# Performance work log

Hardware: AMD Instinct MI355X
Metric: run time of the kernel (lower is better)

The kernel has to match this reference:

```python
import jax, jax.numpy as jnp
import numpy as np

N_NODES = 3000
N_FEAT = 2
N_UNITS = 64
BATCH = 16
K_DIFF = 2  # max_diffusion_step


def _supports(adj):
    # dual_random_walk: (D^-1 A)^T and (D'^-1 A^T)^T, rows with zero degree -> 0
    def rw_T(A):
        d = A.sum(axis=1)
        d_inv = jnp.where(d > 0, 1.0 / d, 0.0)
        return (d_inv[:, None] * A).T  # (N, N)
    return [rw_T(adj), rw_T(adj.T)]


def _gconv(inputs, state, supports, W, b, num_nodes):
    # inputs: (B, N*F), state: (B, N*U)
    B = inputs.shape[0]
    x = jnp.concatenate([inputs.reshape(B, num_nodes, -1),
                         state.reshape(B, num_nodes, -1)], axis=2)  # (B, N, C)
    x0 = x.transpose(1, 2, 0)  # (N, C, B)
    mats = [x0]
    for S in supports:
        x1 = jnp.einsum('mn,ncb->mcb', S, x0)
        mats.append(x1)
        xk_1, xk_2 = x1, x0
        for _ in range(2, K_DIFF + 1):
            x2 = 2.0 * jnp.einsum('mn,ncb->mcb', S, xk_1) - xk_2  # Chebyshev recurrence
            mats.append(x2)
            xk_1, xk_2 = x2, xk_1
    xs = jnp.stack(mats, axis=0)  # (M, N, C, B)
    M, _, C, _ = xs.shape
    xs = xs.transpose(3, 1, 2, 0).reshape(B * num_nodes, C * M)
    out = xs @ W + b  # (B*N, O)
    return out.reshape(B, num_nodes * W.shape[1])


def setup_inputs() -> dict:
    key = jax.random.key(0)
    k1, k2, k3, k4, k5 = jax.random.split(key, 5)
    C = N_FEAT + N_UNITS          # 66
    M = 2 * K_DIFF + 1            # 5 (two supports)
    xw = lambda k, s: jax.random.normal(k, s, dtype=jnp.float32) * jnp.sqrt(2.0 / (s[0] + s[1]))
    return {
        "inputs": jax.random.normal(k1, (BATCH, N_NODES * N_FEAT), dtype=jnp.float32),
        "hx": jax.random.normal(k2, (BATCH, N_NODES * N_UNITS), dtype=jnp.float32),
        "adj_mx": jax.random.uniform(k3, (N_NODES, N_NODES), dtype=jnp.float32),
        "W_gate": xw(k4, (C * M, 2 * N_UNITS)),
        "b_gate": jnp.ones((2 * N_UNITS,), dtype=jnp.float32),  # bias_start=1.0
        "W_cand": xw(k5, (C * M, N_UNITS)),
        "b_cand": jnp.zeros((N_UNITS,), dtype=jnp.float32),
        "num_nodes": N_NODES,
    }


def reference(inputs, hx, adj_mx, W_gate, b_gate, W_cand, b_cand, num_nodes):
    supports = _supports(adj_mx)
    B = inputs.shape[0]
    value = jax.nn.sigmoid(_gconv(inputs, hx, supports, W_gate, b_gate, num_nodes))
    value = value.reshape(B, num_nodes, 2 * N_UNITS)
    r, u = value[..., :N_UNITS], value[..., N_UNITS:]
    r = r.reshape(B, num_nodes * N_UNITS)
    u = u.reshape(B, num_nodes * N_UNITS)
    c = jnp.tanh(_gconv(inputs, r * hx, supports, W_cand, b_cand, num_nodes))
    new_state = u * hx + (1.0 - u) * c
    return new_state
```

## Files before the change

kernel.cpp:

```cpp
#include <hip/hip_runtime.h>
#include <cstdint>
#include <cstddef>


typedef unsigned short u16;
typedef __bf16 bf16x8 __attribute__((ext_vector_type(8)));
typedef u16 u16x8 __attribute__((ext_vector_type(8)));
typedef float f32x4 __attribute__((ext_vector_type(4)));

#define NND 3000
#define KP  3008
#define NBX 16
#define NCB 1056
#define KW  330
#define KWP 352

__device__ __forceinline__ float b2f(u16 x) { return (float)__builtin_bit_cast(__bf16, x); }
__device__ __forceinline__ u16 f2b(float f) { return __builtin_bit_cast(u16, (__bf16)f); }

__device__ __forceinline__ void gll16(const u16* g, void* l) {
  __builtin_amdgcn_global_load_lds(
      (const __attribute__((address_space(1))) unsigned int*)g,
      (__attribute__((address_space(3))) unsigned int*)l, 16, 0, 0);
}


__global__ void k_probe(const u16* __restrict__ bg, int* __restrict__ flag) {
  if (threadIdx.x == 0 && blockIdx.x == 0) *flag = (bg[0] == 0x3F80) ? 0 : 1;
}

__device__ __forceinline__ float rdf(const void* p, size_t i, int mode) {
  return mode ? ((const float*)p)[i] : b2f(((const u16*)p)[i]);
}


__global__ __launch_bounds__(256) void k_rowsum(const void* __restrict__ A, float* __restrict__ d0inv,
                                                const int* __restrict__ flag) {
  const int row = blockIdx.x, t = threadIdx.x;
  const int mode = *flag;
  float s = 0.f;
  if (mode) {
    const float* a = (const float*)A + (size_t)row * NND;
    for (int j = t; j < NND; j += 256) s += a[j];
  } else {
    const u16* a = (const u16*)A + (size_t)row * NND;
    for (int j = t; j < NND; j += 256) s += b2f(a[j]);
  }
  for (int off = 32; off; off >>= 1) s += __shfl_down(s, off, 64);
  __shared__ float red[4];
  if ((t & 63) == 0) red[t >> 6] = s;
  __syncthreads();
  if (t == 0) {
    float tot = red[0] + red[1] + red[2] + red[3];
    d0inv[row] = tot > 0.f ? 1.f / tot : 0.f;
  }
}

__global__ __launch_bounds__(256) void k_colsum(const void* __restrict__ A, float* __restrict__ d1sum,
                                                const int* __restrict__ flag) {
  const int j = blockIdx.x * 256 + threadIdx.x;
  if (j >= NND) return;
  const int mode = *flag;
  const int i0 = blockIdx.y * 100;
  float s = 0.f;
  if (mode) {
    const float* a = (const float*)A;
    for (int i = i0; i < i0 + 100; ++i) s += a[(size_t)i * NND + j];
  } else {
    const u16* a = (const u16*)A;
    for (int i = i0; i < i0 + 100; ++i) s += b2f(a[(size_t)i * NND + j]);
  }
  atomicAdd(&d1sum[j], s);
}

__global__ __launch_bounds__(256) void k_sboth(const void* __restrict__ A, const float* __restrict__ d0inv,
                                               const float* __restrict__ d1sum,
                                               u16* __restrict__ S0, u16* __restrict__ S1,
                                               const int* __restrict__ flag) {
  __shared__ float ldsx[64 * 65];
  __shared__ float inv1c[64];
  __shared__ float inv0r[64];
  const int C = blockIdx.x * 64, R = blockIdx.y * 64, t = threadIdx.x;
  const int mode = *flag;
  if (t < 64) {
    int cg = C + t;
    float ds = (cg < NND) ? d1sum[cg] : 0.f;
    inv1c[t] = ds > 0.f ? 1.f / ds : 0.f;
  } else if (t < 128) {
    int rg = R + (t - 64);
    inv0r[t - 64] = (rg < NND) ? d0inv[rg] : 0.f;
  }
#pragma unroll
  for (int ph = 0; ph < 16; ++ph) {
    int idx = t + ph * 256;
    int r = idx >> 6, c = idx & 63;
    int rg = R + r, cg = C + c;
    ldsx[r * 65 + c] = (rg < NND && cg < NND) ? rdf(A, (size_t)rg * NND + cg, mode) : 0.f;
  }
  __syncthreads();
#pragma unroll
  for (int ph = 0; ph < 16; ++ph) {
    int idx = t + ph * 256;
    int mr = idx >> 6, nc = idx & 63;
    int m1 = R + mr, n1 = C + nc;
    if (m1 < NND && n1 < KP)
      S1[(size_t)m1 * KP + n1] = f2b(ldsx[mr * 65 + nc] * inv1c[nc]);
    int m0_ = C + mr, n0_ = R + nc;
    if (m0_ < NND && n0_ < KP)
      S0[(size_t)m0_ * KP + n0_] = f2b(ldsx[nc * 65 + mr] * inv0r[nc]);
  }
}

__global__ __launch_bounds__(256) void k_wt2(const void* __restrict__ Wg, const void* __restrict__ Wc,
                                             u16* __restrict__ Wtg, u16* __restrict__ Wtc,
                                             const int* __restrict__ flag) {
  const int idx = blockIdx.x * 256 + threadIdx.x;
  const int mode = *flag;
  if (idx < 128 * KWP) {
    int o = idx / KWP, k = idx - o * KWP;
    float v = (k < KW) ? rdf(Wg, (size_t)k * 128 + o, mode) : 0.f;
    Wtg[idx] = f2b(v);
  } else if (idx < 192 * KWP) {
    int i2 = idx - 128 * KWP;
    int o = i2 / KWP, k = i2 - o * KWP;
    float v = (k < KW) ? rdf(Wc, (size_t)k * 64 + o, mode) : 0.f;
    Wtc[i2] = f2b(v);
  }
}

__global__ __launch_bounds__(256) void k_buildx(const void* __restrict__ inp, const void* __restrict__ hx,
                                                u16* __restrict__ xtg, u16* __restrict__ xtc,
                                                u16* __restrict__ chx, const int* __restrict__ flag) {
  __shared__ __align__(16) u16 hxl[128 * 72];
  const int nt = blockIdx.x, b = blockIdx.y;
  const int n0 = nt * 128, t = threadIdx.x;
  const int mode = *flag;
#pragma unroll
  for (int i = 0; i < 4; ++i) {
    int id = t + 256 * i;
    int nl = id >> 3, og = (id & 7) * 8;
    int ng = n0 + nl; if (ng > NND - 1) ng = NND - 1;
    const size_t base = (size_t)b * 192000 + (size_t)ng * 64 + og;
    u16x8 v;
    if (mode) {
      const float* h = (const float*)hx + base;
      f32x4 lo = *(const f32x4*)h, hi = *(const f32x4*)(h + 4);
      v[0] = f2b(lo[0]); v[1] = f2b(lo[1]); v[2] = f2b(lo[2]); v[3] = f2b(lo[3]);
      v[4] = f2b(hi[0]); v[5] = f2b(hi[1]); v[6] = f2b(hi[2]); v[7] = f2b(hi[3]);
    } else {
      v = *(const u16x8*)&((const u16*)hx)[base];
    }
    *(u16x8*)&hxl[nl * 72 + og] = v;
  }
  __syncthreads();
#pragma unroll
  for (int i = 0; i < 4; ++i) {
    int id = t + 256 * i;
    int nl = id >> 3, og = (id & 7) * 8;
    int ng = n0 + nl;
    if (ng < NND)
      *(u16x8*)&chx[(size_t)b * 192000 + (size_t)ng * 64 + og] = *(u16x8*)&hxl[nl * 72 + og];
  }
#pragma unroll
  for (int i = 0; i < 4; ++i) {
    int id = t + 256 * i;
    int u = id >> 4, ngrp = (id & 15) * 8;
    int nb = n0 + ngrp;
    if (nb < KP) {
      u16x8 v;
#pragma unroll
      for (int e = 0; e < 8; ++e) {
        int ng = nb + e;
        v[e] = (ng < NND) ? hxl[(ngrp + e) * 72 + u] : (u16)0;
      }
      *(u16x8*)&xtg[(size_t)((2 + u) * 16 + b) * KP + nb] = v;
    }
  }
  if (t < 32) {
    int c = t >> 4, ngrp = (t & 15) * 8;
    int nb = n0 + ngrp;
    if (nb < KP) {
      u16x8 v;
#pragma unroll
      for (int e = 0; e < 8; ++e) {
        int ng = nb + e;
        v[e] = (ng < NND) ? f2b(rdf(inp, (size_t)b * 6000 + (size_t)ng * 2 + c, mode)) : (u16)0;
      }
      *(u16x8*)&xtg[(size_t)(c * 16 + b) * KP + nb] = v;
      *(u16x8*)&xtc[(size_t)(c * 16 + b) * KP + nb] = v;
    }
  }
  if (nt == 23 && t < 64) {
    u16x8 z = {0, 0, 0, 0, 0, 0, 0, 0};
    *(u16x8*)&xtc[(size_t)((2 + t) * 16 + b) * KP + NND] = z;
  }
}

struct GemmAParams {
  const u16* A0; const u16* A1;
  const u16* B0; const u16* B1;
  u16* D0; u16* D1;
  const u16* X;
  int mode;
};

__global__ __launch_bounds__(256, 3) void k_gemmA(GemmAParams p) {
  __shared__ __align__(16) u16 lds[24576];
  const int bid = blockIdx.x;
  const int x8 = bid & 7, g = bid >> 3;
  const int slot = g / 11, n_idx = g - slot * 11;
  const int strip = x8 * 8 + slot;
  const int m_idx = strip >> 1, z = strip & 1;
  const u16* Sp = z ? p.A1 : p.A0;
  const u16* Bp = z ? p.B1 : p.B0;
  u16* Dp = z ? p.D1 : p.D0;
  const int n0 = n_idx * 96;
  const int m0 = m_idx * 96;
  const int t = threadIdx.x;
  const int lane = t & 63, w = t >> 6;
  const int wr = w >> 1, wc = w & 1;
  const int l15 = lane & 15, lq = lane >> 4;
  const int x7 = l15 & 7;

  const u16* gsrc[6];
  int lbase[6];
#pragma unroll
  for (int q = 0; q < 6; ++q) {
    const int c = t + 256 * q;
    if (c < 768) {
      const int row = c >> 3, grp = c & 7;
      int mg = m0 + row; if (mg > NND - 1) mg = NND - 1;
      gsrc[q] = Sp + (size_t)mg * KP + ((grp ^ (row & 7)) << 3);
      lbase[q] = q * 4096 + w * 1024;
    } else {
      const int c2 = c - 768;
      const int row = c2 >> 3, grp = c2 & 7;
      gsrc[q] = Bp + (size_t)(n0 + row) * KP + ((grp ^ (row & 7)) << 3);
      lbase[q] = 12288 + (q - 3) * 4096 + w * 1024;
    }
  }

  f32x4 acc[3][3];
#pragma unroll
  for (int i = 0; i < 3; ++i)
#pragma unroll
    for (int j = 0; j < 3; ++j) acc[i][j] = (f32x4){0.f, 0.f, 0.f, 0.f};

  auto STAGE = [&](int buf) {
    char* L = (char*)lds + buf * 24576;
#pragma unroll
    for (int q = 0; q < 6; ++q) { gll16(gsrc[q], (void*)(L + lbase[q])); gsrc[q] += 64; }
  };
  auto STEP = [&](int buf) {
    const u16* L = lds + buf * 12288;
    bf16x8 af[3][2], bf[3][2];
#pragma unroll
    for (int kk = 0; kk < 2; ++kk) {
#pragma unroll
      for (int i = 0; i < 3; ++i)
        af[i][kk] = *(const bf16x8*)&L[(wr * 48 + i * 16 + l15) * 64 + (((kk * 4 + lq) ^ x7) << 3)];
#pragma unroll
      for (int j = 0; j < 3; ++j)
        bf[j][kk] = *(const bf16x8*)&L[6144 + (wc * 48 + j * 16 + l15) * 64 + (((kk * 4 + lq) ^ x7) << 3)];
    }
#pragma unroll
    for (int kk = 0; kk < 2; ++kk)
#pragma unroll
      for (int i = 0; i < 3; ++i)
#pragma unroll
        for (int j = 0; j < 3; ++j)
          acc[i][j] = __builtin_amdgcn_mfma_f32_16x16x32_bf16(af[i][kk], bf[j][kk], acc[i][j], 0, 0, 0);
  };

  STAGE(0);
  for (int ks = 0; ks < 47; ++ks) {
    const int buf = ks & 1;
    if (ks < 46) {
      STAGE(buf ^ 1);
      asm volatile("s_waitcnt vmcnt(6)" ::: "memory");
    } else {
      asm volatile("s_waitcnt vmcnt(0)" ::: "memory");
    }
    __builtin_amdgcn_s_barrier();
    __builtin_amdgcn_sched_barrier(0);
    STEP(buf);
    __builtin_amdgcn_sched_barrier(0);
    __builtin_amdgcn_s_barrier();
  }

  __syncthreads();
  u16* Tw = &lds[w * 3456];
#pragma unroll
  for (int i = 0; i < 3; ++i)
#pragma unroll
    for (int j = 0; j < 3; ++j)
#pragma unroll
      for (int r = 0; r < 4; ++r) {
        int miw = i * 16 + lq * 4 + r;
        int niw = j * 16 + l15;
        float v = acc[i][j][r];
        if (m0 + wr * 48 + miw >= NND) v = 0.f;
        Tw[niw * 56 + miw] = f2b(v);
      }
  const int row8 = lane >> 3, colg8 = lane & 7;
#pragma unroll
  for (int ph = 0; ph < 6; ++ph) {
    int nrow = ph * 8 + row8;
    int n_g = n0 + wc * 48 + nrow;
    int m_b = m0 + wr * 48 + colg8 * 8;
    if (colg8 < 6 && m_b < KP) {
      u16x8 y = *(u16x8*)&Tw[nrow * 56 + colg8 * 8];
      if (p.mode) {
        const u16x8 x = *(const u16x8*)&p.X[(size_t)n_g * KP + m_b];
#pragma unroll
        for (int e = 0; e < 8; ++e) y[e] = f2b(2.f * b2f(y[e]) - b2f(x[e]));
      }
      *(u16x8*)&Dp[(size_t)n_g * KP + m_b] = y;
    }
  }
}

struct GateParams {
  const u16* xall;
  const u16* Wt;
  const void* bias;
  const u16* hx;
  u16* xtc;
  u16* ut;
  const int* flag;
};

__global__ __launch_bounds__(256, 2) void k_gate(GateParams p) {
  __shared__ __align__(16) u16 Al[128 * 40];
  __shared__ __align__(16) u16 Bl[64 * 40];
  __shared__ __align__(16) u16 hxl[64 * 72];
  __shared__ int rowA[KWP];
  const int b = blockIdx.y, n0 = blockIdx.x * 64;
  const int t = threadIdx.x, lane = t & 63, w = t >> 6, wr = w >> 1, wc = w & 1;
  const int l15 = lane & 15, lq = lane >> 4;
  const int mode = *p.flag;

  for (int k = t; k < KWP; k += 256) {
    int c = k / 5, mt = k - c * 5;
    rowA[k] = (k < KW) ? (mt * NCB + c * 16 + b) * KP : 0;
  }
#pragma unroll
  for (int i = 0; i < 2; ++i) {
    int id = t + 256 * i;
    int nl = id >> 3, og = (id & 7) * 8;
    int ng = n0 + nl; if (ng > NND - 1) ng = NND - 1;
    *(u16x8*)&hxl[nl * 72 + og] = *(const u16x8*)&p.hx[(size_t)b * 192000 + (size_t)ng * 64 + og];
  }
  __syncthreads();

  f32x4 acc[4][2];
#pragma unroll
  for (int i = 0; i < 4; ++i)
#pragma unroll
    for (int j = 0; j < 2; ++j) acc[i][j] = (f32x4){0.f, 0.f, 0.f, 0.f};

  u16x8 aReg[2]; u16x8 bReg;
#pragma unroll
  for (int hh = 0; hh < 2; ++hh) {
    int id = t + 256 * hh;
    int r = id >> 2, g = id & 3;
    aReg[hh] = *(const u16x8*)&p.Wt[(size_t)r * KWP + g * 8];
  }
#pragma unroll
  for (int e = 0; e < 8; ++e) {
    int k = w * 8 + e;
    u16 x = p.xall[(size_t)rowA[k] + n0 + lane];
    bReg[e] = (k < KW) ? x : (u16)0;
  }

  for (int ks = 0; ks < 11; ++ks) {
    __syncthreads();
#pragma unroll
    for (int hh = 0; hh < 2; ++hh) {
      int id = t + 256 * hh;
      int r = id >> 2, g = id & 3;
      *(u16x8*)&Al[r * 40 + g * 8] = aReg[hh];
    }
    *(u16x8*)&Bl[lane * 40 + w * 8] = bReg;
    __syncthreads();

    if (ks + 1 < 11) {
      const int k0 = (ks + 1) * 32;
#pragma unroll
      for (int hh = 0; hh < 2; ++hh) {
        int id = t + 256 * hh;
        int r = id >> 2, g = id & 3;
        aReg[hh] = *(const u16x8*)&p.Wt[(size_t)r * KWP + k0 + g * 8];
      }
#pragma unroll
      for (int e = 0; e < 8; ++e) {
        int k = k0 + w * 8 + e;
        u16 x = p.xall[(size_t)rowA[k] + n0 + lane];
        bReg[e] = (k < KW) ? x : (u16)0;
      }
    }

    bf16x8 af[4], bf[2];
#pragma unroll
    for (int i = 0; i < 4; ++i) af[i] = *(const bf16x8*)&Al[(wr * 64 + i * 16 + l15) * 40 + lq * 8];
#pragma unroll
    for (int j = 0; j < 2; ++j) bf[j] = *(const bf16x8*)&Bl[(wc * 32 + j * 16 + l15) * 40 + lq * 8];
#pragma unroll
    for (int i = 0; i < 4; ++i)
#pragma unroll
      for (int j = 0; j < 2; ++j)
        acc[i][j] = __builtin_amdgcn_mfma_f32_16x16x32_bf16(af[i], bf[j], acc[i][j], 0, 0, 0);
  }

#pragma unroll
  for (int i = 0; i < 4; ++i)
#pragma unroll
    for (int j = 0; j < 2; ++j)
#pragma unroll
      for (int r = 0; r < 4; ++r) {
        int o = wr * 64 + i * 16 + lq * 4 + r;
        int nl = wc * 32 + j * 16 + l15;
        int ng = n0 + nl;
        if (ng < NND) {
          float v = acc[i][j][r] + rdf(p.bias, o, mode);
          float s = 1.f / (1.f + __expf(-v));
          if (o < 64) {
            float rh = s * b2f(hxl[nl * 72 + o]);
            p.xtc[(size_t)((o + 2) * 16 + b) * KP + ng] = f2b(rh);
          } else {
            p.ut[(size_t)b * 192000 + (size_t)(o - 64) * NND + ng] = f2b(s);
          }
        }
      }
}

struct CandParams {
  const u16* xall;
  const u16* Wt;
  const void* bias;
  const u16* hx;
  const u16* ut;
  void* out;
  const int* flag;
};

__global__ __launch_bounds__(256, 2) void k_cand(CandParams p) {
  __shared__ __align__(16) u16 Al[64 * 40];
  __shared__ __align__(16) u16 Bl[64 * 40];
  __shared__ __align__(16) u16 hxl[64 * 72];
  __shared__ __align__(16) u16 newl[64 * 72];
  __shared__ int rowA[KWP];
  const int b = blockIdx.y, n0 = blockIdx.x * 64;
  const int t = threadIdx.x, lane = t & 63, w = t >> 6, wr = w >> 1, wc = w & 1;
  const int l15 = lane & 15, lq = lane >> 4;
  const int mode = *p.flag;

  for (int k = t; k < KWP; k += 256) {
    int c = k / 5, mt = k - c * 5;
    rowA[k] = (k < KW) ? (mt * NCB + c * 16 + b) * KP : 0;
  }
#pragma unroll
  for (int i = 0; i < 2; ++i) {
    int id = t + 256 * i;
    int nl = id >> 3, og = (id & 7) * 8;
    int ng = n0 + nl; if (ng > NND - 1) ng = NND - 1;
    *(u16x8*)&hxl[nl * 72 + og] = *(const u16x8*)&p.hx[(size_t)b * 192000 + (size_t)ng * 64 + og];
  }
  __syncthreads();

  f32x4 acc[2][2];
#pragma unroll
  for (int i = 0; i < 2; ++i)
#pragma unroll
    for (int j = 0; j < 2; ++j) acc[i][j] = (f32x4){0.f, 0.f, 0.f, 0.f};

  u16x8 aReg; u16x8 bReg;
  {
    int r = t >> 2, g = t & 3;
    aReg = *(const u16x8*)&p.Wt[(size_t)r * KWP + g * 8];
  }
#pragma unroll
  for (int e = 0; e < 8; ++e) {
    int k = w * 8 + e;
    u16 x = p.xall[(size_t)rowA[k] + n0 + lane];
    bReg[e] = (k < KW) ? x : (u16)0;
  }

  for (int ks = 0; ks < 11; ++ks) {
    __syncthreads();
    {
      int r = t >> 2, g = t & 3;
      *(u16x8*)&Al[r * 40 + g * 8] = aReg;
    }
    *(u16x8*)&Bl[lane * 40 + w * 8] = bReg;
    __syncthreads();

    if (ks + 1 < 11) {
      const int k0 = (ks + 1) * 32;
      {
        int r = t >> 2, g = t & 3;
        aReg = *(const u16x8*)&p.Wt[(size_t)r * KWP + k0 + g * 8];
      }
#pragma unroll
      for (int e = 0; e < 8; ++e) {
        int k = k0 + w * 8 + e;
        u16 x = p.xall[(size_t)rowA[k] + n0 + lane];
        bReg[e] = (k < KW) ? x : (u16)0;
      }
    }

    bf16x8 af[2], bf[2];
#pragma unroll
    for (int i = 0; i < 2; ++i) af[i] = *(const bf16x8*)&Al[(wr * 32 + i * 16 + l15) * 40 + lq * 8];
#pragma unroll
    for (int j = 0; j < 2; ++j) bf[j] = *(const bf16x8*)&Bl[(wc * 32 + j * 16 + l15) * 40 + lq * 8];
#pragma unroll
    for (int i = 0; i < 2; ++i)
#pragma unroll
      for (int j = 0; j < 2; ++j)
        acc[i][j] = __builtin_amdgcn_mfma_f32_16x16x32_bf16(af[i], bf[j], acc[i][j], 0, 0, 0);
  }

#pragma unroll
  for (int i = 0; i < 2; ++i)
#pragma unroll
    for (int j = 0; j < 2; ++j)
#pragma unroll
      for (int r = 0; r < 4; ++r) {
        int o = wr * 32 + i * 16 + lq * 4 + r;
        int nl = wc * 32 + j * 16 + l15;
        int ng = n0 + nl; int ngc = ng > NND - 1 ? NND - 1 : ng;
        float v = acc[i][j][r] + rdf(p.bias, o, mode);
        float c = tanhf(v);
        float u = b2f(p.ut[(size_t)b * 192000 + (size_t)o * NND + ngc]);
        float h = b2f(hxl[nl * 72 + o]);
        newl[nl * 72 + o] = f2b(u * h + (1.f - u) * c);
      }
  __syncthreads();
#pragma unroll
  for (int i = 0; i < 2; ++i) {
    int id = t + 256 * i;
    int nl = id >> 3, og = (id & 7) * 8;
    int ng = n0 + nl;
    if (ng < NND) {
      u16x8 v = *(u16x8*)&newl[nl * 72 + og];
      if (mode) {
        float* of = (float*)p.out + (size_t)b * 192000 + (size_t)ng * 64 + og;
        f32x4 lo = {b2f(v[0]), b2f(v[1]), b2f(v[2]), b2f(v[3])};
        f32x4 hi = {b2f(v[4]), b2f(v[5]), b2f(v[6]), b2f(v[7])};
        *(f32x4*)of = lo;
        *(f32x4*)(of + 4) = hi;
      } else {
        *(u16x8*)&((u16*)p.out)[(size_t)b * 192000 + (size_t)ng * 64 + og] = v;
      }
    }
  }
}


extern "C" void kernel_launch(void* const* d_in, const int* in_sizes, int n_in,
                              void* d_out, int out_size, void* d_ws, size_t ws_size,
                              hipStream_t stream) {
  const size_t SL = (size_t)NCB * KP;
  size_t off = 0;
  auto alloc = [&](size_t bytes) {
    void* pp = (char*)d_ws + off;
    off += (bytes + 255) & ~(size_t)255;
    return pp;
  };
  u16* S0  = (u16*)alloc((size_t)NND * KP * 2);
  u16* S1  = (u16*)alloc((size_t)NND * KP * 2);
  u16* Xg  = (u16*)alloc(5 * SL * 2);
  u16* Xc  = (u16*)alloc(5 * SL * 2);
  u16* Ut  = (u16*)alloc((size_t)NBX * 64 * NND * 2);
  u16* Wtg = (u16*)alloc((size_t)128 * KWP * 2);
  u16* Wtc = (u16*)alloc((size_t)64 * KWP * 2);
  float* d0inv = (float*)alloc(NND * 4);
  float* d1sum = (float*)alloc(NND * 4);
  u16* cHx  = (u16*)alloc((size_t)3072000 * 2);
  int* flag = (int*)alloc(256);
  (void)in_sizes; (void)n_in; (void)out_size;

  if (ws_size < off) return;

  u16* Xtg = Xg;            u16* Y1 = Xg + SL;  u16* Z2 = Xg + 2 * SL;
  u16* Y3 = Xg + 3 * SL;    u16* Z4 = Xg + 4 * SL;
  u16* Xtc = Xc;            u16* Y1c = Xc + SL; u16* Z2c = Xc + 2 * SL;
  u16* Y3c = Xc + 3 * SL;   u16* Z4c = Xc + 4 * SL;

  const void* inp = d_in[0];
  const void* hx  = d_in[1];
  const void* adj = d_in[2];
  const void* Wg  = d_in[3];
  const void* bg  = d_in[4];
  const void* Wc  = d_in[5];
  const void* bc  = d_in[6];

  k_probe<<<1, 64, 0, stream>>>((const u16*)bg, flag);
  hipMemsetAsync(d1sum, 0, NND * 4, stream);
  k_rowsum<<<NND, 256, 0, stream>>>(adj, d0inv, flag);
  k_colsum<<<dim3(12, 30), 256, 0, stream>>>(adj, d1sum, flag);
  k_sboth<<<dim3(47, 47), 256, 0, stream>>>(adj, d0inv, d1sum, S0, S1, flag);
  k_wt2<<<264, 256, 0, stream>>>(Wg, Wc, Wtg, Wtc, flag);
  k_buildx<<<dim3(24, NBX), 256, 0, stream>>>(inp, hx, Xtg, Xtc, cHx, flag);

  GemmAParams g1 = {S0, S1, Xtg, Xtg, Y1, Y3, nullptr, 0};
  k_gemmA<<<704, 256, 0, stream>>>(g1);
  GemmAParams g2 = {S0, S1, Y1, Y3, Z2, Z4, Xtg, 1};
  k_gemmA<<<704, 256, 0, stream>>>(g2);

  GateParams gp = {Xg, Wtg, bg, cHx, Xtc, Ut, flag};
  k_gate<<<dim3(47, NBX), 256, 0, stream>>>(gp);

  GemmAParams g3 = {S0, S1, Xtc, Xtc, Y1c, Y3c, nullptr, 0};
  k_gemmA<<<704, 256, 0, stream>>>(g3);
  GemmAParams g4 = {S0, S1, Y1c, Y3c, Z2c, Z4c, Xtc, 1};
  k_gemmA<<<704, 256, 0, stream>>>(g4);

  CandParams cp = {Xc, Wtc, bc, cHx, Ut, d_out, flag};
  k_cand<<<dim3(47, NBX), 256, 0, stream>>>(cp);
}
```

Baseline: 403.7 us.

## Enlarge diffusion GEMM tiles to 128x128 and fuse row/column degree sums

The diffusion GEMM tiles grow from 96x96 to 128x128, giving each wave a 4x4 MFMA block. The grid becomes 432 blocks with 2 blocks per CU instead of 3, and the X slabs are padded to 1152 columns so that n-tiles of 128 fit. This raises arithmetic intensity per LDS load and cuts the number of blocks, but lowers occupancy. Separately, the row-sum and column-sum kernels are merged into one tiled kernel that reads the adjacency once and accumulates both degree sums with atomics.

After: 371.4 us. 8.0% less time.

```diff
diff --git a/kernel.cpp b/kernel.cpp
--- a/kernel.cpp
+++ b/kernel.cpp
@@ -12,6 +12,7 @@
 #define KP  3008
 #define NBX 16
 #define NCB 1056
+#define NCBP 1152
 #define KW  330
 #define KWP 352
 
@@ -34,46 +35,40 @@
 }
 
 
-__global__ __launch_bounds__(256) void k_rowsum(const void* __restrict__ A, float* __restrict__ d0inv,
-                                                const int* __restrict__ flag) {
-  const int row = blockIdx.x, t = threadIdx.x;
+__global__ __launch_bounds__(256) void k_sums(const void* __restrict__ A,
+                                              float* __restrict__ d0sum, float* __restrict__ d1sum,
+                                              const int* __restrict__ flag) {
+  __shared__ float ldsx[64 * 65];
+  const int C = blockIdx.x * 64, R = blockIdx.y * 64, t = threadIdx.x;
   const int mode = *flag;
-  float s = 0.f;
-  if (mode) {
-    const float* a = (const float*)A + (size_t)row * NND;
-    for (int j = t; j < NND; j += 256) s += a[j];
-  } else {
-    const u16* a = (const u16*)A + (size_t)row * NND;
-    for (int j = t; j < NND; j += 256) s += b2f(a[j]);
-  }
-  for (int off = 32; off; off >>= 1) s += __shfl_down(s, off, 64);
-  __shared__ float red[4];
-  if ((t & 63) == 0) red[t >> 6] = s;
+#pragma unroll
+  for (int ph = 0; ph < 16; ++ph) {
+    int idx = t + ph * 256;
+    int r = idx >> 6, c = idx & 63;
+    int rg = R + r, cg = C + c;
+    ldsx[r * 65 + c] = (rg < NND && cg < NND) ? rdf(A, (size_t)rg * NND + cg, mode) : 0.f;
+  }
   __syncthreads();
-  if (t == 0) {
-    float tot = red[0] + red[1] + red[2] + red[3];
-    d0inv[row] = tot > 0.f ? 1.f / tot : 0.f;
-  }
-}
-
-__global__ __launch_bounds__(256) void k_colsum(const void* __restrict__ A, float* __restrict__ d1sum,
-                                                const int* __restrict__ flag) {
-  const int j = blockIdx.x * 256 + threadIdx.x;
-  if (j >= NND) return;
-  const int mode = *flag;
-  const int i0 = blockIdx.y * 100;
-  float s = 0.f;
-  if (mode) {
-    const float* a = (const float*)A;
-    for (int i = i0; i < i0 + 100; ++i) s += a[(size_t)i * NND + j];
-  } else {
-    const u16* a = (const u16*)A;
-    for (int i = i0; i < i0 + 100; ++i) s += b2f(a[(size_t)i * NND + j]);
-  }
-  atomicAdd(&d1sum[j], s);
-}
-
-__global__ __launch_bounds__(256) void k_sboth(const void* __restrict__ A, const float* __restrict__ d0inv,
+  if (t < 64) {
+    int rg = R + t;
+    if (rg < NND) {
+      float s = 0.f;
+#pragma unroll 8
+      for (int c = 0; c < 64; ++c) s += ldsx[t * 65 + c];
+      atomicAdd(&d0sum[rg], s);
+    }
+  } else if (t < 128) {
+    int cg = C + (t - 64);
+    if (cg < NND) {
+      float s = 0.f;
+#pragma unroll 8
+      for (int r = 0; r < 64; ++r) s += ldsx[r * 65 + (t - 64)];
+      atomicAdd(&d1sum[cg], s);
+    }
+  }
+}
+
+__global__ __launch_bounds__(256) void k_sboth(const void* __restrict__ A, const float* __restrict__ d0sum,
                                                const float* __restrict__ d1sum,
                                                u16* __restrict__ S0, u16* __restrict__ S1,
                                                const int* __restrict__ flag) {
@@ -88,7 +83,8 @@
     inv1c[t] = ds > 0.f ? 1.f / ds : 0.f;
   } else if (t < 128) {
     int rg = R + (t - 64);
-    inv0r[t - 64] = (rg < NND) ? d0inv[rg] : 0.f;
+    float ds = (rg < NND) ? d0sum[rg] : 0.f;
+    inv0r[t - 64] = ds > 0.f ? 1.f / ds : 0.f;
   }
 #pragma unroll
   for (int ph = 0; ph < 16; ++ph) {
@@ -204,71 +200,71 @@
   int mode;
 };
 
-__global__ __launch_bounds__(256, 3) void k_gemmA(GemmAParams p) {
-  __shared__ __align__(16) u16 lds[24576];
+__global__ __launch_bounds__(256, 2) void k_gemmA(GemmAParams p) {
+  __shared__ __align__(16) u16 lds[32768];
   const int bid = blockIdx.x;
   const int x8 = bid & 7, g = bid >> 3;
-  const int slot = g / 11, n_idx = g - slot * 11;
-  const int strip = x8 * 8 + slot;
+  const int slot = g / 9, n_idx = g - slot * 9;
+  const int strip = x8 * 6 + slot;
   const int m_idx = strip >> 1, z = strip & 1;
   const u16* Sp = z ? p.A1 : p.A0;
   const u16* Bp = z ? p.B1 : p.B0;
   u16* Dp = z ? p.D1 : p.D0;
-  const int n0 = n_idx * 96;
-  const int m0 = m_idx * 96;
+  const int n0 = n_idx * 128;
+  const int m0 = m_idx * 128;
   const int t = threadIdx.x;
   const int lane = t & 63, w = t >> 6;
   const int wr = w >> 1, wc = w & 1;
   const int l15 = lane & 15, lq = lane >> 4;
   const int x7 = l15 & 7;
 
-  const u16* gsrc[6];
-  int lbase[6];
-#pragma unroll
-  for (int q = 0; q < 6; ++q) {
+  const u16* gsrc[8];
+  int lbase[8];
+#pragma unroll
+  for (int q = 0; q < 8; ++q) {
     const int c = t + 256 * q;
-    if (c < 768) {
+    if (c < 1024) {
       const int row = c >> 3, grp = c & 7;
       int mg = m0 + row; if (mg > NND - 1) mg = NND - 1;
       gsrc[q] = Sp + (size_t)mg * KP + ((grp ^ (row & 7)) << 3);
       lbase[q] = q * 4096 + w * 1024;
     } else {
-      const int c2 = c - 768;
+      const int c2 = c - 1024;
       const int row = c2 >> 3, grp = c2 & 7;
       gsrc[q] = Bp + (size_t)(n0 + row) * KP + ((grp ^ (row & 7)) << 3);
-      lbase[q] = 12288 + (q - 3) * 4096 + w * 1024;
-    }
-  }
-
-  f32x4 acc[3][3];
-#pragma unroll
-  for (int i = 0; i < 3; ++i)
-#pragma unroll
-    for (int j = 0; j < 3; ++j) acc[i][j] = (f32x4){0.f, 0.f, 0.f, 0.f};
+      lbase[q] = 16384 + (q - 4) * 4096 + w * 1024;
+    }
+  }
+
+  f32x4 acc[4][4];
+#pragma unroll
+  for (int i = 0; i < 4; ++i)
+#pragma unroll
+    for (int j = 0; j < 4; ++j) acc[i][j] = (f32x4){0.f, 0.f, 0.f, 0.f};
 
   auto STAGE = [&](int buf) {
-    char* L = (char*)lds + buf * 24576;
-#pragma unroll
-    for (int q = 0; q < 6; ++q) { gll16(gsrc[q], (void*)(L + lbase[q])); gsrc[q] += 64; }
+    char* L = (char*)lds + buf * 32768;
+#pragma unroll
+    for (int q = 0; q < 8; ++q) { gll16(gsrc[q], (void*)(L + lbase[q])); gsrc[q] += 64; }
   };
   auto STEP = [&](int buf) {
-    const u16* L = lds + buf * 12288;
-    bf16x8 af[3][2], bf[3][2];
+    const u16* L = lds + buf * 16384;
+    bf16x8 af[4][2], bf[4][2];
 #pragma unroll
     for (int kk = 0; kk < 2; ++kk) {
 #pragma unroll
-      for (int i = 0; i < 3; ++i)
-        af[i][kk] = *(const bf16x8*)&L[(wr * 48 + i * 16 + l15) * 64 + (((kk * 4 + lq) ^ x7) << 3)];
-#pragma unroll
-      for (int j = 0; j < 3; ++j)
-        bf[j][kk] = *(const bf16x8*)&L[6144 + (wc * 48 + j * 16 + l15) * 64 + (((kk * 4 + lq) ^ x7) << 3)];
+      for (int i = 0; i < 4; ++i)
+        af[i][kk] = *(const bf16x8*)&L[(wr * 64 + i * 16 + l15) * 64 + (((kk * 4 + lq) ^ x7) << 3)];
+#pragma unroll
+      for (int j = 0; j < 4; ++j)
+        bf[j][kk] = *(const bf16x8*)&L[8192 + (wc * 64 + j * 16 + l15) * 64 + (((kk * 4 + lq) ^ x7) << 3)];
     }
 #pragma unroll
     for (int kk = 0; kk < 2; ++kk)
 #pragma unroll
-      for (int i = 0; i < 3; ++i)
-#pragma unroll
-        for (int j = 0; j < 3; ++j)
+      for (int i = 0; i < 4; ++i)
+#pragma unroll
+        for (int j = 0; j < 4; ++j)
           acc[i][j] = __builtin_amdgcn_mfma_f32_16x16x32_bf16(af[i][kk], bf[j][kk], acc[i][j], 0, 0, 0);
   };
 
@@ -277,7 +273,7 @@
     const int buf = ks & 1;
     if (ks < 46) {
       STAGE(buf ^ 1);
-      asm volatile("s_waitcnt vmcnt(6)" ::: "memory");
+      asm volatile("s_waitcnt vmcnt(8)" ::: "memory");
     } else {
       asm volatile("s_waitcnt vmcnt(0)" ::: "memory");
     }
@@ -289,27 +285,27 @@
   }
 
   __syncthreads();
-  u16* Tw = &lds[w * 3456];
-#pragma unroll
-  for (int i = 0; i < 3; ++i)
-#pragma unroll
-    for (int j = 0; j < 3; ++j)
+  u16* Tw = &lds[w * 4608];
+#pragma unroll
+  for (int i = 0; i < 4; ++i)
+#pragma unroll
+    for (int j = 0; j < 4; ++j)
 #pragma unroll
       for (int r = 0; r < 4; ++r) {
         int miw = i * 16 + lq * 4 + r;
         int niw = j * 16 + l15;
         float v = acc[i][j][r];
-        if (m0 + wr * 48 + miw >= NND) v = 0.f;
-        Tw[niw * 56 + miw] = f2b(v);
-      }
-  const int row8 = lane >> 3, colg8 = lane & 7;
-#pragma unroll
-  for (int ph = 0; ph < 6; ++ph) {
+        if (m0 + wr * 64 + miw >= NND) v = 0.f;
+        Tw[niw * 72 + miw] = f2b(v);
+      }
+  const int row8 = lane >> 3, colg = (lane & 7) * 8;
+#pragma unroll
+  for (int ph = 0; ph < 8; ++ph) {
     int nrow = ph * 8 + row8;
-    int n_g = n0 + wc * 48 + nrow;
-    int m_b = m0 + wr * 48 + colg8 * 8;
-    if (colg8 < 6 && m_b < KP) {
-      u16x8 y = *(u16x8*)&Tw[nrow * 56 + colg8 * 8];
+    int n_g = n0 + wc * 64 + nrow;
+    int m_b = m0 + wr * 64 + colg;
+    if (m_b < KP) {
+      u16x8 y = *(u16x8*)&Tw[nrow * 72 + colg];
       if (p.mode) {
         const u16x8 x = *(const u16x8*)&p.X[(size_t)n_g * KP + m_b];
 #pragma unroll
@@ -342,7 +338,7 @@
 
   for (int k = t; k < KWP; k += 256) {
     int c = k / 5, mt = k - c * 5;
-    rowA[k] = (k < KW) ? (mt * NCB + c * 16 + b) * KP : 0;
+    rowA[k] = (k < KW) ? (mt * NCBP + c * 16 + b) * KP : 0;
   }
 #pragma unroll
   for (int i = 0; i < 2; ++i) {
@@ -457,7 +453,7 @@
 
   for (int k = t; k < KWP; k += 256) {
     int c = k / 5, mt = k - c * 5;
-    rowA[k] = (k < KW) ? (mt * NCB + c * 16 + b) * KP : 0;
+    rowA[k] = (k < KW) ? (mt * NCBP + c * 16 + b) * KP : 0;
   }
 #pragma unroll
   for (int i = 0; i < 2; ++i) {
@@ -561,7 +557,7 @@
 extern "C" void kernel_launch(void* const* d_in, const int* in_sizes, int n_in,
                               void* d_out, int out_size, void* d_ws, size_t ws_size,
                               hipStream_t stream) {
-  const size_t SL = (size_t)NCB * KP;
+  const size_t SLP = (size_t)NCBP * KP;
   size_t off = 0;
   auto alloc = [&](size_t bytes) {
     void* pp = (char*)d_ws + off;
@@ -570,23 +566,25 @@
   };
   u16* S0  = (u16*)alloc((size_t)NND * KP * 2);
   u16* S1  = (u16*)alloc((size_t)NND * KP * 2);
-  u16* Xg  = (u16*)alloc(5 * SL * 2);
-  u16* Xc  = (u16*)alloc(5 * SL * 2);
+  u16* Xg  = (u16*)alloc(5 * SLP * 2);
+  u16* Xc  = (u16*)alloc(5 * SLP * 2);
   u16* Ut  = (u16*)alloc((size_t)NBX * 64 * NND * 2);
   u16* Wtg = (u16*)alloc((size_t)128 * KWP * 2);
   u16* Wtc = (u16*)alloc((size_t)64 * KWP * 2);
-  float* d0inv = (float*)alloc(NND * 4);
-  float* d1sum = (float*)alloc(NND * 4);
+  float* dsums = (float*)alloc(2 * NND * 4);
   u16* cHx  = (u16*)alloc((size_t)3072000 * 2);
   int* flag = (int*)alloc(256);
   (void)in_sizes; (void)n_in; (void)out_size;
 
   if (ws_size < off) return;
 
-  u16* Xtg = Xg;            u16* Y1 = Xg + SL;  u16* Z2 = Xg + 2 * SL;
-  u16* Y3 = Xg + 3 * SL;    u16* Z4 = Xg + 4 * SL;
-  u16* Xtc = Xc;            u16* Y1c = Xc + SL; u16* Z2c = Xc + 2 * SL;
-  u16* Y3c = Xc + 3 * SL;   u16* Z4c = Xc + 4 * SL;
+  float* d0sum = dsums;
+  float* d1sum = dsums + NND;
+
+  u16* Xtg = Xg;            u16* Y1 = Xg + SLP;  u16* Z2 = Xg + 2 * SLP;
+  u16* Y3 = Xg + 3 * SLP;   u16* Z4 = Xg + 4 * SLP;
+  u16* Xtc = Xc;            u16* Y1c = Xc + SLP; u16* Z2c = Xc + 2 * SLP;
+  u16* Y3c = Xc + 3 * SLP;  u16* Z4c = Xc + 4 * SLP;
 
   const void* inp = d_in[0];
   const void* hx  = d_in[1];
@@ -597,25 +595,24 @@
   const void* bc  = d_in[6];
 
   k_probe<<<1, 64, 0, stream>>>((const u16*)bg, flag);
-  hipMemsetAsync(d1sum, 0, NND * 4, stream);
-  k_rowsum<<<NND, 256, 0, stream>>>(adj, d0inv, flag);
-  k_colsum<<<dim3(12, 30), 256, 0, stream>>>(adj, d1sum, flag);
-  k_sboth<<<dim3(47, 47), 256, 0, stream>>>(adj, d0inv, d1sum, S0, S1, flag);
+  hipMemsetAsync(dsums, 0, 2 * NND * 4, stream);
+  k_sums<<<dim3(47, 47), 256, 0, stream>>>(adj, d0sum, d1sum, flag);
+  k_sboth<<<dim3(47, 47), 256, 0, stream>>>(adj, d0sum, d1sum, S0, S1, flag);
   k_wt2<<<264, 256, 0, stream>>>(Wg, Wc, Wtg, Wtc, flag);
   k_buildx<<<dim3(24, NBX), 256, 0, stream>>>(inp, hx, Xtg, Xtc, cHx, flag);
 
   GemmAParams g1 = {S0, S1, Xtg, Xtg, Y1, Y3, nullptr, 0};
-  k_gemmA<<<704, 256, 0, stream>>>(g1);
+  k_gemmA<<<432, 256, 0, stream>>>(g1);
   GemmAParams g2 = {S0, S1, Y1, Y3, Z2, Z4, Xtg, 1};
-  k_gemmA<<<704, 256, 0, stream>>>(g2);
+  k_gemmA<<<432, 256, 0, stream>>>(g2);
 
   GateParams gp = {Xg, Wtg, bg, cHx, Xtc, Ut, flag};
   k_gate<<<dim3(47, NBX), 256, 0, stream>>>(gp);
 
   GemmAParams g3 = {S0, S1, Xtc, Xtc, Y1c, Y3c, nullptr, 0};
-  k_gemmA<<<704, 256, 0, stream>>>(g3);
+  k_gemmA<<<432, 256, 0, stream>>>(g3);
   GemmAParams g4 = {S0, S1, Y1c, Y3c, Z2c, Z4c, Xtc, 1};
-  k_gemmA<<<704, 256, 0, stream>>>(g4);
+  k_gemmA<<<432, 256, 0, stream>>>(g4);
 
   CandParams cp = {Xc, Wtc, bc, cHx, Ut, d_out, flag};
   k_cand<<<dim3(47, NBX), 256, 0, stream>>>(cp);
```
